# Optimization experiments

Measured on AMD Instinct MI355X. Metric: run time of the kernel, lower is better.

## Reference

```python
import jax, jax.numpy as jnp
import numpy as np

B, T, D, H = 4, 2048, 1024, 16
S = D // H  # head dim

def setup_inputs() -> dict:
    key = jax.random.key(0)
    kx, kq, ku, kb = jax.random.split(key, 4)
    x = jax.random.normal(kx, (B, T, D), dtype=jnp.float32)
    # torch nn.Linear weights: (out, in); y = x @ W.T
    Wq = jax.random.normal(kq, (D, D), dtype=jnp.float32) * (1.0 / np.sqrt(D))
    Wu = jax.random.normal(ku, (D, D), dtype=jnp.float32) * (1.0 / np.sqrt(D))
    bu = jax.random.normal(kb, (D,), dtype=jnp.float32) * 0.01
    return {"x": x, "Wq": Wq, "Wu": Wu, "bu": bu}

def reference(x, Wq, Wu, bu):
    b, t, k = x.shape
    h, s = H, S
    # Bug in original module replicated: Q, K, V all use to_queries.
    q = x @ Wq.T  # (b,t,k)
    qh = q.reshape(b, t, h, s).transpose(0, 2, 1, 3)  # (b,h,t,s)
    scores = jnp.einsum('bhts,bhus->bhtu', qh, qh) / jnp.sqrt(jnp.asarray(s, x.dtype))
    w = jax.nn.softmax(scores, axis=-1)  # (b,h,t,t)
    out = jnp.einsum('bhtu,bhus->bhts', w, qh)  # (b,h,t,s)
    out = out.transpose(0, 2, 1, 3).reshape(b, t, k)  # merge heads
    return out @ Wu.T + bu
```

## Files before the change

### kernel.cpp

```cpp
#include <hip/hip_runtime.h>

#define B_ 4
#define T_ 2048
#define D_ 1024
#define H_ 16
#define S_ 64

typedef __attribute__((ext_vector_type(8))) short bf16x8;
typedef __attribute__((ext_vector_type(16))) float f32x16;
typedef unsigned int uint;

__device__ __forceinline__ short f2bf(float f) {
    union { float f; uint u; } v; v.f = f;
    uint r = v.u + 0x7fffu + ((v.u >> 16) & 1u);
    return (short)(r >> 16);
}

__device__ __forceinline__ void gld16(const short* g, short* l) {
    __builtin_amdgcn_global_load_lds((const __attribute__((address_space(1))) void*)g,
                                     (__attribute__((address_space(3))) void*)l, 16, 0, 0);
}

__global__ __launch_bounds__(256) void cvt3(const float* __restrict__ x,
                                            const float* __restrict__ wq,
                                            const float* __restrict__ wu,
                                            short* __restrict__ xb,
                                            short* __restrict__ wqb,
                                            short* __restrict__ wub) {
    const int NX = B_ * T_ * D_ / 8;
    const int NW = D_ * D_ / 8;
    int i = blockIdx.x * 256 + threadIdx.x;
    const float* src; short* dst; int off;
    if (i < NX)            { src = x;  dst = xb;  off = i; }
    else if (i < NX + NW)  { src = wq; dst = wqb; off = i - NX; }
    else                   { src = wu; dst = wub; off = i - NX - NW; }
    float4 a = *(const float4*)(src + (size_t)off * 8);
    float4 b = *(const float4*)(src + (size_t)off * 8 + 4);
    short o[8] = {f2bf(a.x), f2bf(a.y), f2bf(a.z), f2bf(a.w),
                  f2bf(b.x), f2bf(b.y), f2bf(b.z), f2bf(b.w)};
    *(bf16x8*)(dst + (size_t)off * 8) = *(bf16x8*)o;
}

#define STAGE_CO(t, bi) do {                                                      \
        const int kk_ = (t) << 6;                                                 \
        const short* gp_ = (wv < 2) ? Ap : Bp;                                    \
        short* lp_ = (wv < 2) ? &As[bi][0] : &Bs[bi][0];                          \
        const int half_ = wv & 1;                                                 \
        _Pragma("unroll")                                                         \
        for (int c_ = 0; c_ < 8; ++c_) {                                          \
            const int r8_  = half_ * 8 + c_;               \
            const int row_ = r8_ * 8 + (lane >> 3);                               \
            const int cs_  = (lane & 7) ^ (lane >> 3);    \
            gld16(gp_ + (size_t)row_ * K + kk_ + cs_ * 8, lp_ + r8_ * 512);       \
        }                                                                         \
    } while (0)

template <bool OUT_BF16>
__global__ __launch_bounds__(256, 2) void gemm_bt(const short* __restrict__ A,
                                                  const short* __restrict__ Bt,
                                                  const float* __restrict__ bias,
                                                  void* __restrict__ Cv,
                                                  int M, int N, int K) {
    __shared__ short As[2][8192];
    __shared__ short Bs[2][8192];
    const int tid  = threadIdx.x;
    const int lane = tid & 63;
    const int wv   = tid >> 6;
    const int wm   = wv >> 1;
    const int wn   = wv & 1;
    const int h32  = lane >> 5;

    int bx = blockIdx.x, by = blockIdx.y;
    {
        const int nbx = gridDim.x, nby = gridDim.y;
        if ((nby & 7) == 0) {
            int f = blockIdx.x + nbx * blockIdx.y;
            int xcd = f & 7, slot = f >> 3;
            bx = slot % nbx;
            by = xcd * (nby >> 3) + slot / nbx;
        }
    }
    const int m0 = by * 128, n0 = bx * 128;
    const short* Ap = A + (size_t)m0 * K;
    const short* Bp = Bt + (size_t)n0 * K;

    f32x16 acc[2][2];
    #pragma unroll
    for (int i = 0; i < 2; ++i)
        #pragma unroll
        for (int j = 0; j < 2; ++j)
            #pragma unroll
            for (int r = 0; r < 16; ++r) acc[i][j][r] = 0.f;

    const int ra0 = wm * 64 + (lane & 31);
    const int rb0 = wn * 64 + (lane & 31);
    const int l7  = lane & 7;

    const int nt = K >> 6;
    STAGE_CO(0, 0);

    for (int t = 0; t < nt; ++t) {
        const int cur = t & 1;
        asm volatile("s_waitcnt vmcnt(0)" ::: "memory");
        __builtin_amdgcn_s_barrier();
        asm volatile("" ::: "memory");

        if (t + 1 < nt) STAGE_CO(t + 1, cur ^ 1);

        const short* Ab = As[cur];
        const short* Bb = Bs[cur];
        #pragma unroll
        for (int ks = 0; ks < 4; ++ks) {
            const int kk8 = ks * 2 + h32;
            const int sl  = (kk8 ^ l7) * 8;
            bf16x8 a0 = *(bf16x8*)&Ab[ra0 * 64 + sl];
            bf16x8 a1 = *(bf16x8*)&Ab[(ra0 + 32) * 64 + sl];
            bf16x8 b0 = *(bf16x8*)&Bb[rb0 * 64 + sl];
            bf16x8 b1 = *(bf16x8*)&Bb[(rb0 + 32) * 64 + sl];
            acc[0][0] = __builtin_amdgcn_mfma_f32_32x32x16_bf16(a0, b0, acc[0][0], 0, 0, 0);
            acc[0][1] = __builtin_amdgcn_mfma_f32_32x32x16_bf16(a0, b1, acc[0][1], 0, 0, 0);
            acc[1][0] = __builtin_amdgcn_mfma_f32_32x32x16_bf16(a1, b0, acc[1][0], 0, 0, 0);
            acc[1][1] = __builtin_amdgcn_mfma_f32_32x32x16_bf16(a1, b1, acc[1][1], 0, 0, 0);
        }
    }

    #pragma unroll
    for (int mt = 0; mt < 2; ++mt) {
        #pragma unroll
        for (int nt2 = 0; nt2 < 2; ++nt2) {
            const int rbase = m0 + wm * 64 + mt * 32;
            const int col   = n0 + wn * 64 + nt2 * 32 + (lane & 31);
            float bv = 0.f;
            if (!OUT_BF16 && bias) bv = bias[col];
            #pragma unroll
            for (int r = 0; r < 16; ++r) {
                int row = rbase + (r & 3) + 8 * (r >> 2) + 4 * h32;
                if constexpr (OUT_BF16)
                    ((short*)Cv)[(size_t)row * N + col] = f2bf(acc[mt][nt2][r]);
                else
                    ((float*)Cv)[(size_t)row * N + col] = acc[mt][nt2][r] + bv;
            }
        }
    }
}

__global__ __launch_bounds__(256, 3) void attn_mfma(const short* __restrict__ q,
                                                    short* __restrict__ o) {
    __shared__ short smem[20480];
    const int tid  = threadIdx.x;
    const int lane = tid & 63;
    const int wv   = tid >> 6;
    const int h32  = lane >> 5;
    const int b  = blockIdx.y >> 4;
    const int hh = blockIdx.y & 15;
    const int t0 = blockIdx.x * 128;
    const short* qb = q + (size_t)b * (T_ * D_) + hh * S_;

    const int c8  = tid & 7;
    const int uu0 = tid >> 3;
    const int uu1 = uu0 + 32;
    const int u_0 = (uu0 & 0x33) | ((uu0 & 4) << 1) | ((uu0 & 8) >> 1);
    const int u_1 = (uu1 & 0x33) | ((uu1 & 4) << 1) | ((uu1 & 8) >> 1);
    const int kfo0 = (c8 * 64 + (u_0 ^ c8)) * 8;
    const int kfo1 = (c8 * 64 + (u_1 ^ c8)) * 8;
    const int kto0 = 4096 + (u_0 >> 4) * 1536 + ((u_0 >> 2) & 1) * 768 + (c8 >> 2) * 8
                   + ((u_0 & 3) | (((u_0 >> 3) & 1) << 2)) + (c8 & 3) * 24;
    const int kto1 = 4096 + (u_1 >> 4) * 1536 + ((u_1 >> 2) & 1) * 768 + (c8 >> 2) * 8
                   + ((u_1 & 3) | (((u_1 >> 3) & 1) << 2)) + (c8 & 3) * 24;
    const short* g0 = qb + (size_t)u_0 * D_ + c8 * 8;
    const short* g1 = qb + (size_t)u_1 * D_ + c8 * 8;

    bf16x8 st0 = *(const bf16x8*)g0;
    bf16x8 st1 = *(const bf16x8*)g1;
    #pragma unroll
    for (int rep = 0; rep < 4; ++rep) {
        int f = rep * 256 + tid;
        int r = f >> 3, cq = f & 7;
        bf16x8 v = *(const bf16x8*)(qb + (size_t)(t0 + r) * D_ + cq * 8);
        *(bf16x8*)&smem[(cq * 128 + (r ^ cq)) * 8] = v;
    }
    __syncthreads();
    bf16x8 Qreg[4];
    #pragma unroll
    for (int ks = 0; ks < 4; ++ks) {
        int kk8 = 2 * ks + h32;
        Qreg[ks] = *(bf16x8*)&smem[(kk8 * 128 + ((wv * 32 + (lane & 31)) ^ kk8)) * 8];
    }
    __syncthreads();
    *(bf16x8*)&smem[kfo0] = st0;
    *(bf16x8*)&smem[kfo1] = st1;
    #pragma unroll
    for (int ds = 0; ds < 8; ++ds) {
        smem[kto0 + ds * 96] = st0[ds];
        smem[kto1 + ds * 96] = st1[ds];
    }
    st0 = *(const bf16x8*)(g0 + (size_t)64 * D_);
    st1 = *(const bf16x8*)(g1 + (size_t)64 * D_);

    f32x16 accO0, accO1;
    #pragma unroll
    for (int i = 0; i < 16; ++i) { accO0[i] = 0.f; accO1[i] = 0.f; }
    float lsp0 = 0.f, lsp1 = 0.f;
    const int prow = ((((lane & 7) << 2) | ((lane >> 3) & 3)) * 24) + h32 * 768;
    const float SCL = 0.18033688f;

    int rb = 0;
    for (int u0 = 0; u0 < T_; u0 += 64) {
        __syncthreads();
        const int wb = 10240 - rb;

        f32x16 aS0, aS1;
        #pragma unroll
        for (int i = 0; i < 16; ++i) { aS0[i] = 0.f; aS1[i] = 0.f; }
        __builtin_amdgcn_s_setprio(1);
        #pragma unroll
        for (int ks = 0; ks < 4; ++ks) {
            int kk8 = 2 * ks + h32;
            bf16x8 k0 = *(bf16x8*)&smem[rb + (kk8 * 64 + ((lane & 31) ^ kk8)) * 8];
            bf16x8 k1 = *(bf16x8*)&smem[rb + (kk8 * 64 + ((32 + (lane & 31)) ^ kk8)) * 8];
            aS0 = __builtin_amdgcn_mfma_f32_32x32x16_bf16(k0, Qreg[ks], aS0, 0, 0, 0);
            aS1 = __builtin_amdgcn_mfma_f32_32x32x16_bf16(k1, Qreg[ks], aS1, 0, 0, 0);
        }
        __builtin_amdgcn_s_setprio(0);

        *(bf16x8*)&smem[wb + kfo0] = st0;
        *(bf16x8*)&smem[wb + kfo1] = st1;
        #pragma unroll
        for (int ds = 0; ds < 8; ++ds) {
            smem[wb + kto0 + ds * 96] = st0[ds];
            smem[wb + kto1 + ds * 96] = st1[ds];
        }
        int un = u0 + 128; if (un >= T_) un = 0;
        st0 = *(const bf16x8*)(g0 + (size_t)un * D_);
        st1 = *(const bf16x8*)(g1 + (size_t)un * D_);

        bf16x8 af[4];
        #pragma unroll
        for (int tt = 0; tt < 2; ++tt) {
            const f32x16& a = tt ? aS1 : aS0;
            float p[16];
            #pragma unroll
            for (int r = 0; r < 16; r += 2) {
                p[r]     = __builtin_amdgcn_exp2f(a[r] * SCL);
                p[r + 1] = __builtin_amdgcn_exp2f(a[r + 1] * SCL);
                lsp0 += p[r];
                lsp1 += p[r + 1];
            }
            #pragma unroll
            for (int sub = 0; sub < 2; ++sub) {
                union { uint u[4]; bf16x8 v; } cv;
                #pragma unroll
                for (int dd = 0; dd < 4; ++dd)
                    cv.u[dd] = __builtin_amdgcn_perm(
                        __float_as_uint(p[sub * 8 + 2 * dd + 1]),
                        __float_as_uint(p[sub * 8 + 2 * dd]), 0x07060302u);
                af[tt * 2 + sub] = cv.v;
            }
        }

        __builtin_amdgcn_s_setprio(1);
        #pragma unroll
        for (int c = 0; c < 4; ++c) {
            bf16x8 v0 = *(bf16x8*)&smem[rb + 4096 + c * 1536 + prow + 0];
            bf16x8 v1 = *(bf16x8*)&smem[rb + 4096 + c * 1536 + prow + 8];
            accO0 = __builtin_amdgcn_mfma_f32_32x32x16_bf16(af[c], v0, accO0, 0, 0, 0);
            accO1 = __builtin_amdgcn_mfma_f32_32x32x16_bf16(af[c], v1, accO1, 0, 0, 0);
        }
        __builtin_amdgcn_s_setprio(0);
        rb = wb;
    }

    float lsp = lsp0 + lsp1;
    float dsum = lsp + __shfl_xor(lsp, 32);
    short* ob = o + (size_t)b * (T_ * D_) + hh * S_;
    #pragma unroll
    for (int r = 0; r < 16; ++r) {
        int rt = (r & 3) + 8 * (r >> 2) + 4 * h32;
        float inv = 1.00390625f / __shfl(dsum, rt);
        size_t t = (size_t)(t0 + wv * 32 + rt);
        ob[t * D_ + (lane & 31)]      = f2bf(accO0[r] * inv);
        ob[t * D_ + 32 + (lane & 31)] = f2bf(accO1[r] * inv);
    }
}

extern "C" void kernel_launch(void* const* d_in, const int* in_sizes, int n_in,
                              void* d_out, int out_size, void* d_ws, size_t ws_size,
                              hipStream_t stream) {
    const float* x  = (const float*)d_in[0];
    const float* Wq = (const float*)d_in[1];
    const float* Wu = (const float*)d_in[2];
    const float* bu = (const float*)d_in[3];
    float* out  = (float*)d_out;
    short* qbuf = (short*)d_out;
    short* xb   = (short*)((char*)d_out + 16777216);
    short* attn = (short*)d_ws;
    short* wqb  = (short*)((char*)d_ws + 16777216);
    short* wub  = (short*)((char*)d_ws + 18874368);

    const int M = B_ * T_;
    dim3 gg(D_ / 128, M / 128);
    hipLaunchKernelGGL(cvt3, dim3(5120), dim3(256), 0, stream, x, Wq, Wu, xb, wqb, wub);
    hipLaunchKernelGGL((gemm_bt<true>), gg, dim3(256), 0, stream,
                       xb, wqb, (const float*)nullptr, (void*)qbuf, M, D_, D_);
    hipLaunchKernelGGL(attn_mfma, dim3(T_ / 128, B_ * H_), dim3(256), 0, stream, qbuf, attn);
    hipLaunchKernelGGL((gemm_bt<false>), gg, dim3(256), 0, stream,
                       attn, wub, bu, (void*)out, M, D_, D_);
}
```

Measured before the change: 223.2 us.

## Stage GEMM tiles through registers with two-ahead prefetch instead of direct LDS loads

```diff
diff --git a/kernel.cpp b/kernel.cpp
--- a/kernel.cpp
+++ b/kernel.cpp
@@ -41,17 +41,22 @@
     *(bf16x8*)(dst + (size_t)off * 8) = *(bf16x8*)o;
 }
 
-#define STAGE_CO(t, bi) do {                                                      \
+#define LOADR(t) do {                                                             \
         const int kk_ = (t) << 6;                                                 \
-        const short* gp_ = (wv < 2) ? Ap : Bp;                                    \
-        short* lp_ = (wv < 2) ? &As[bi][0] : &Bs[bi][0];                          \
-        const int half_ = wv & 1;                                                 \
         _Pragma("unroll")                                                         \
-        for (int c_ = 0; c_ < 8; ++c_) {                                          \
-            const int r8_  = half_ * 8 + c_;               \
-            const int row_ = r8_ * 8 + (lane >> 3);                               \
-            const int cs_  = (lane & 7) ^ (lane >> 3);    \
-            gld16(gp_ + (size_t)row_ * K + kk_ + cs_ * 8, lp_ + r8_ * 512);       \
+        for (int j_ = 0; j_ < 4; ++j_) {                                          \
+            stA[j_] = *(const bf16x8*)(Ap + (size_t)(row0 + 32 * j_) * K + kk_ + c7 * 8); \
+            stB[j_] = *(const bf16x8*)(Bp + (size_t)(row0 + 32 * j_) * K + kk_ + c7 * 8); \
+        }                                                                         \
+    } while (0)
+
+#define WRITEL(bi) do {                                                           \
+        _Pragma("unroll")                                                         \
+        for (int j_ = 0; j_ < 4; ++j_) {                                          \
+            const int r_ = row0 + 32 * j_;                                        \
+            const int s_ = (r_ * 8 + (c7 ^ (r_ & 7))) * 8;                        \
+            *(bf16x8*)&As[bi][s_] = stA[j_];                                      \
+            *(bf16x8*)&Bs[bi][s_] = stB[j_];                                      \
         }                                                                         \
     } while (0)
 
@@ -69,6 +74,8 @@
     const int wm   = wv >> 1;
     const int wn   = wv & 1;
     const int h32  = lane >> 5;
+    const int row0 = tid >> 3;
+    const int c7   = tid & 7;
 
     int bx = blockIdx.x, by = blockIdx.y;
     {
@@ -96,16 +103,23 @@
     const int rb0 = wn * 64 + (lane & 31);
     const int l7  = lane & 7;
 
+    bf16x8 stA[4], stB[4];
     const int nt = K >> 6;
-    STAGE_CO(0, 0);
+
+    LOADR(0);
+    asm volatile("s_waitcnt vmcnt(0)" ::: "memory");
+    WRITEL(0);
+    if (nt > 1) LOADR(1);
+    __syncthreads();
 
     for (int t = 0; t < nt; ++t) {
         const int cur = t & 1;
-        asm volatile("s_waitcnt vmcnt(0)" ::: "memory");
+        asm volatile("s_waitcnt vmcnt(0) lgkmcnt(0)" ::: "memory");
         __builtin_amdgcn_s_barrier();
         asm volatile("" ::: "memory");
 
-        if (t + 1 < nt) STAGE_CO(t + 1, cur ^ 1);
+        if (t + 1 < nt) WRITEL(cur ^ 1);
+        if (t + 2 < nt) LOADR(t + 2);
 
         const short* Ab = As[cur];
         const short* Bb = Bs[cur];
```

Result: no change. 225.9 us (+1.2%).
